# Kernel optimization log

Hardware: AMD Instinct MI355X
Metric: run time of the kernel (lower is better)

## Reference

```python
import jax, jax.numpy as jnp
import numpy as np

N_NODES = 50000
EMBED_DIM = 128
HIDDEN_DIM = 64
N_EDGES = 1600000
TEMP = 1.0


def setup_inputs() -> dict:
    key = jax.random.key(0)
    k1, k2, k3, k4 = jax.random.split(key, 4)
    node_embed = jax.random.normal(k1, (N_NODES, EMBED_DIM), dtype=jnp.float32)
    edge_index = jax.random.randint(k2, (2, N_EDGES), 0, N_NODES, dtype=jnp.int64)
    # MLP params (Linear(2*D, H) -> ReLU -> Linear(H, 1)); PyTorch-style fan-in scaling
    W1 = jax.random.normal(k3, (2 * EMBED_DIM, HIDDEN_DIM), dtype=jnp.float32) * (1.0 / np.sqrt(2 * EMBED_DIM))
    b1 = jnp.zeros((HIDDEN_DIM,), dtype=jnp.float32)
    W2 = jax.random.normal(k4, (HIDDEN_DIM, 1), dtype=jnp.float32) * (1.0 / np.sqrt(HIDDEN_DIM))
    b2 = jnp.zeros((1,), dtype=jnp.float32)
    return {"node_embed": node_embed, "edge_index": edge_index,
            "W1": W1, "b1": b1, "W2": W2, "b2": b2}


def reference(node_embed, edge_index, W1, b1, W2, b2):
    row, col = edge_index[0], edge_index[1]
    # gather + concat: [E, 2*D]
    edge_feat = jnp.concatenate([node_embed[row], node_embed[col]], axis=1)
    # tiny 2-layer MLP (dropout = identity in eval mode)
    h = jax.nn.relu(edge_feat @ W1 + b1)            # [E, H]
    edge_logits = (h @ W2 + b2)[:, 0]               # [E]
    # gumbel-sigmoid: difference of two Gumbel(0,1) samples (= logistic noise)
    nk = jax.random.key(42)
    nk1, nk2 = jax.random.split(nk)
    noise = jax.random.gumbel(nk1, edge_logits.shape, dtype=edge_logits.dtype) \
          - jax.random.gumbel(nk2, edge_logits.shape, dtype=edge_logits.dtype)
    edge_probs = jax.nn.sigmoid((edge_logits + noise) / TEMP)
    return edge_probs
```

## Files before the change

kernel.cpp:

```cpp
#include <hip/hip_runtime.h>
#include <hip/hip_bf16.h>
#include <stdint.h>

#define N_NODES 50000
#define NE      1600000
#define DIM     128
#define HID     64

typedef __attribute__((ext_vector_type(8))) short bf16x8;
typedef __attribute__((ext_vector_type(4))) float f32x4;

struct TF2 { uint32_t a, b; };

__host__ __device__ constexpr uint32_t rotl32(uint32_t x, int d) {
  return (x << d) | (x >> (32 - d));
}

__host__ __device__ constexpr TF2 threefry(uint32_t k0, uint32_t k1,
                                           uint32_t c0, uint32_t c1) {
  uint32_t ks[3] = { k0, k1, k0 ^ k1 ^ 0x1BD11BDAu };
  uint32_t x0 = c0 + ks[0], x1 = c1 + ks[1];
  const int rot[2][4] = { {13, 15, 26, 6}, {17, 29, 16, 24} };
  for (int i = 0; i < 5; ++i) {
    for (int r = 0; r < 4; ++r) {
      x0 += x1;
      x1 = rotl32(x1, rot[i & 1][r]);
      x1 ^= x0;
    }
    x0 += ks[(i + 1) % 3];
    x1 += ks[(i + 2) % 3] + (uint32_t)(i + 1);
  }
  return { x0, x1 };
}

constexpr TF2 SPA = threefry(0u, 42u, 0u, 0u);
constexpr TF2 SPB = threefry(0u, 42u, 0u, 1u);
constexpr uint32_t NK1_0 = SPA.a, NK1_1 = SPA.b;
constexpr uint32_t NK2_0 = SPB.a, NK2_1 = SPB.b;

__device__ inline float gumbel_elem(uint32_t k0, uint32_t k1, uint32_t i) {
  TF2 t = threefry(k0, k1, 0u, i);
  uint32_t bits = t.a ^ t.b;
  float f = __uint_as_float((bits >> 9) | 0x3f800000u) - 1.0f;
  float u = fmaxf(1.1754943508222875e-38f, f + 1.1754943508222875e-38f);
  return -__logf(-__logf(u));
}

__device__ inline unsigned short f2bf_rne(float f) {
  uint32_t u = __float_as_uint(f);
  uint32_t r = (u + 0x7fffu + ((u >> 16) & 1u)) >> 16;
  return (unsigned short)r;
}

#define NPB_M  64
#define NBLKN  ((N_NODES + NPB_M - 1) / NPB_M)
#define WT_LD  136

__global__ __launch_bounds__(256, 4)
void node_mfma_kernel(const float* __restrict__ node,
                      const float* __restrict__ W1,
                      const float* __restrict__ b1,
                      unsigned short* __restrict__ A_tab,
                      unsigned short* __restrict__ B_tab) {
  __shared__ unsigned short wt[128 * WT_LD];

  const int tid  = threadIdx.x;
  const int lane = tid & 63;
  const int w    = tid >> 6;
  const int c    = lane & 15;
  const int b    = lane >> 4;
  const int v0   = blockIdx.x * NPB_M;

  for (int idx = tid; idx < 128 * 128; idx += 256) {
    const int k  = idx >> 7;
    const int np = idx & 127;
    const float wv = W1[((size_t)((np >> 6) * 128 + k)) * HID + (np & 63)];
    wt[np * WT_LD + k] = f2bf_rne(wv);
  }
  __syncthreads();

  const int vld = min(v0 + w * 16 + c, N_NODES - 1);
  const float4* __restrict__ xrp = (const float4*)(node + (size_t)vld * DIM);
  float4 xx[8];
#pragma unroll
  for (int kk = 0; kk < 4; ++kk) {
    xx[2 * kk]     = xrp[kk * 8 + b * 2];
    xx[2 * kk + 1] = xrp[kk * 8 + b * 2 + 1];
  }

  f32x4 acc[8];
#pragma unroll
  for (int nt = 0; nt < 8; ++nt) acc[nt] = (f32x4){0.f, 0.f, 0.f, 0.f};

#pragma unroll
  for (int kk = 0; kk < 4; ++kk) {
    const float4 x0 = xx[2 * kk];
    const float4 x1 = xx[2 * kk + 1];
    const float xs[8] = { x0.x, x0.y, x0.z, x0.w, x1.x, x1.y, x1.z, x1.w };
    bf16x8 af;
#pragma unroll
    for (int j = 0; j < 8; ++j) af[j] = (short)f2bf_rne(xs[j]);

#pragma unroll
    for (int nt = 0; nt < 8; ++nt) {
      const bf16x8 bf =
          *(const bf16x8*)&wt[(nt * 16 + c) * WT_LD + kk * 32 + b * 8];
      acc[nt] = __builtin_amdgcn_mfma_f32_16x16x32_bf16(af, bf, acc[nt], 0, 0, 0);
    }
  }

#pragma unroll
  for (int nt = 0; nt < 8; ++nt) {
    const int np = nt * 16 + c;
    const float badd = (np < HID) ? b1[np] : 0.0f;
    unsigned short* __restrict__ base =
        (np < HID) ? (A_tab + np) : (B_tab + (np - HID));
#pragma unroll
    for (int r = 0; r < 4; ++r) {
      const int v = v0 + w * 16 + b * 4 + r;
      if (v < N_NODES) base[(size_t)v * HID] = f2bf_rne(acc[nt][r] + badd);
    }
  }
}

__global__ __launch_bounds__(256, 5)
void edge_kernel(const int* __restrict__ ei,
                 const unsigned short* __restrict__ A_tab,
                 const unsigned short* __restrict__ B_tab,
                 const float* __restrict__ W2,
                 const float* __restrict__ b2,
                 float* __restrict__ out) {
  const int tid    = blockIdx.x * blockDim.x + threadIdx.x;
  const int stride = gridDim.x * blockDim.x;
  const float bias2 = b2[0];

  for (int e = tid; e < NE; e += stride) {
    const int r = __builtin_nontemporal_load(ei + e);
    const int c = __builtin_nontemporal_load(ei + NE + e);
    const uint4* __restrict__ ap = (const uint4*)(A_tab + (size_t)r * HID);
    const uint4* __restrict__ bp = (const uint4*)(B_tab + (size_t)c * HID);

    uint4 av[8], bv[8];
#pragma unroll
    for (int q = 0; q < 8; ++q) av[q] = ap[q];
#pragma unroll
    for (int q = 0; q < 8; ++q) bv[q] = bp[q];

    float logit = bias2;
#pragma unroll
    for (int q = 0; q < 8; ++q) {
      const uint32_t* au = (const uint32_t*)&av[q];
      const uint32_t* bu = (const uint32_t*)&bv[q];
#pragma unroll
      for (int t = 0; t < 4; ++t) {
        const float a0 = __uint_as_float(au[t] << 16);
        const float a1 = __uint_as_float(au[t] & 0xffff0000u);
        const float b0 = __uint_as_float(bu[t] << 16);
        const float b1v = __uint_as_float(bu[t] & 0xffff0000u);
        const int jj = q * 8 + t * 2;
        logit = fmaf(fmaxf(a0 + b0, 0.0f),  W2[jj],     logit);
        logit = fmaf(fmaxf(a1 + b1v, 0.0f), W2[jj + 1], logit);
      }
    }

    const float g1 = gumbel_elem(NK1_0, NK1_1, (uint32_t)e);
    const float g2 = gumbel_elem(NK2_0, NK2_1, (uint32_t)e);
    const float z  = logit + g1 - g2;
    __builtin_nontemporal_store(1.0f / (1.0f + __expf(-z)), out + e);
  }
}

__global__ __launch_bounds__(256, 4)
void edge_prune_fallback(const float* __restrict__ node,
                         const int*   __restrict__ ei,
                         const float* __restrict__ W1,
                         const float* __restrict__ b1,
                         const float* __restrict__ W2,
                         const float* __restrict__ b2,
                         float*       __restrict__ out) {
  const int tid    = blockIdx.x * blockDim.x + threadIdx.x;
  const int stride = gridDim.x * blockDim.x;
  const float bias2 = b2[0];

  for (int e = tid; e < NE; e += stride) {
    const int r = ei[e];
    const int c = ei[NE + e];
    const float4* __restrict__ up = (const float4*)(node + (size_t)r * DIM);
    const float4* __restrict__ vp = (const float4*)(node + (size_t)c * DIM);

    float h[HID];
#pragma unroll
    for (int j = 0; j < HID; ++j) h[j] = b1[j];

#pragma unroll 1
    for (int dd = 0; dd < DIM / 4; ++dd) {
      const float4 xu = up[dd];
      const float4 xv = vp[dd];
      const float xs[8] = { xu.x, xu.y, xu.z, xu.w, xv.x, xv.y, xv.z, xv.w };
#pragma unroll
      for (int k = 0; k < 8; ++k) {
        const int drow = (k < 4) ? (dd * 4 + k) : (DIM + dd * 4 + (k - 4));
        const float4* __restrict__ wrow = (const float4*)(W1 + drow * HID);
        const float x = xs[k];
#pragma unroll
        for (int j4 = 0; j4 < HID / 4; ++j4) {
          const float4 w = wrow[j4];
          h[j4 * 4 + 0] = fmaf(x, w.x, h[j4 * 4 + 0]);
          h[j4 * 4 + 1] = fmaf(x, w.y, h[j4 * 4 + 1]);
          h[j4 * 4 + 2] = fmaf(x, w.z, h[j4 * 4 + 2]);
          h[j4 * 4 + 3] = fmaf(x, w.w, h[j4 * 4 + 3]);
        }
      }
    }

    float logit = bias2;
#pragma unroll
    for (int j = 0; j < HID; ++j) logit = fmaf(fmaxf(h[j], 0.0f), W2[j], logit);

    const float g1 = gumbel_elem(NK1_0, NK1_1, (uint32_t)e);
    const float g2 = gumbel_elem(NK2_0, NK2_1, (uint32_t)e);
    const float z  = logit + g1 - g2;
    out[e] = 1.0f / (1.0f + __expf(-z));
  }
}

extern "C" void kernel_launch(void* const* d_in, const int* in_sizes, int n_in,
                              void* d_out, int out_size, void* d_ws, size_t ws_size,
                              hipStream_t stream) {
  const float* node = (const float*)d_in[0];
  const int*   ei   = (const int*)  d_in[1];
  const float* W1   = (const float*)d_in[2];
  const float* b1   = (const float*)d_in[3];
  const float* W2   = (const float*)d_in[4];
  const float* b2   = (const float*)d_in[5];
  float* out = (float*)d_out;

  const size_t tab_bytes = (size_t)N_NODES * HID * sizeof(unsigned short);
  if (ws_size >= 2 * tab_bytes) {
    unsigned short* A_tab = (unsigned short*)d_ws;
    unsigned short* B_tab = A_tab + (size_t)N_NODES * HID;
    node_mfma_kernel<<<dim3(NBLKN), dim3(256), 0, stream>>>(
        node, W1, b1, A_tab, B_tab);
    edge_kernel<<<dim3(1280), dim3(256), 0, stream>>>(
        ei, A_tab, B_tab, W2, b2, out);
  } else {
    edge_prune_fallback<<<dim3(1024), dim3(256), 0, stream>>>(
        node, ei, W1, b1, W2, b2, out);
  }
}
```

Before: 84.14 us.

## Gather edge table rows into LDS via direct global-to-LDS DMA loads

Rewrites the edge kernel so each wave gathers the bf16 A/B table rows for 64 edges into shared memory with global_load_lds, coalescing one 16-byte segment per lane, using an XOR swizzle to avoid bank conflicts. Gumbel noise is computed while the loads are in flight, then the waits are drained and each lane reads its row from LDS. This replaces per-thread scattered 16-byte register loads with wave-cooperative loads that overlap the RNG arithmetic, at the cost of 64KB LDS per block, lower occupancy (2 blocks/CU) and a smaller grid with no cross-iteration prefetch.

```diff
diff --git a/kernel.cpp b/kernel.cpp
--- a/kernel.cpp
+++ b/kernel.cpp
@@ -123,49 +123,72 @@
   }
 }
 
-__global__ __launch_bounds__(256, 5)
-void edge_kernel(const int* __restrict__ ei,
-                 const unsigned short* __restrict__ A_tab,
-                 const unsigned short* __restrict__ B_tab,
-                 const float* __restrict__ W2,
-                 const float* __restrict__ b2,
-                 float* __restrict__ out) {
-  const int tid    = blockIdx.x * blockDim.x + threadIdx.x;
-  const int stride = gridDim.x * blockDim.x;
+#define EPB    256
+#define NBATCH (NE / EPB)
+
+__global__ __launch_bounds__(256, 2)
+void edge_kernel_dma(const int* __restrict__ ei,
+                     const unsigned short* __restrict__ A_tab,
+                     const unsigned short* __restrict__ B_tab,
+                     const float* __restrict__ W2,
+                     const float* __restrict__ b2,
+                     float* __restrict__ out) {
+  __shared__ uint4 buf[4096];
+
+  const int lane = threadIdx.x & 63;
+  const int w    = threadIdx.x >> 6;
+  const int l7   = lane & 7;
   const float bias2 = b2[0];
 
-  for (int e = tid; e < NE; e += stride) {
-    const int r = __builtin_nontemporal_load(ei + e);
-    const int c = __builtin_nontemporal_load(ei + NE + e);
-    const uint4* __restrict__ ap = (const uint4*)(A_tab + (size_t)r * HID);
-    const uint4* __restrict__ bp = (const uint4*)(B_tab + (size_t)c * HID);
-
-    uint4 av[8], bv[8];
-#pragma unroll
-    for (int q = 0; q < 8; ++q) av[q] = ap[q];
-#pragma unroll
-    for (int q = 0; q < 8; ++q) bv[q] = bp[q];
+  uint4* wbuf = buf + w * 1024;
+
+  for (int bt = blockIdx.x; bt < NBATCH; bt += gridDim.x) {
+    const int e0 = bt * EPB + w * 64;
+
+#pragma unroll
+    for (int j = 0; j < 16; ++j) {
+      const int sgl = j * 64 + lane;
+      const int ed  = sgl >> 4;
+      const int s   = sgl & 15;
+      const int q   = (s & 8) | ((s & 7) ^ (ed & 7));
+      const int idx = __builtin_nontemporal_load(ei + e0 + ed + (q < 8 ? 0 : NE));
+      const unsigned short* g =
+          (q < 8 ? A_tab : B_tab) + (size_t)idx * HID + (q & 7) * 8;
+      __builtin_amdgcn_global_load_lds(
+          (const __attribute__((address_space(1))) uint32_t*)g,
+          (__attribute__((address_space(3))) uint32_t*)(wbuf + j * 64),
+          16, 0, 0);
+    }
+
+    const int e = e0 + lane;
+    const float g1 = gumbel_elem(NK1_0, NK1_1, (uint32_t)e);
+    const float g2 = gumbel_elem(NK2_0, NK2_1, (uint32_t)e);
+
+    asm volatile("s_waitcnt vmcnt(0)" ::: "memory");
+    __builtin_amdgcn_sched_barrier(0);
 
     float logit = bias2;
-#pragma unroll
-    for (int q = 0; q < 8; ++q) {
-      const uint32_t* au = (const uint32_t*)&av[q];
-      const uint32_t* bu = (const uint32_t*)&bv[q];
+    const int tbase = lane * 16;
+#pragma unroll
+    for (int qq = 0; qq < 8; ++qq) {
+      const int slo = qq ^ l7;
+      const uint4 a4 = wbuf[tbase + slo];
+      const uint4 b4 = wbuf[tbase + 8 + slo];
+      const uint32_t* au = (const uint32_t*)&a4;
+      const uint32_t* bu = (const uint32_t*)&b4;
 #pragma unroll
       for (int t = 0; t < 4; ++t) {
         const float a0 = __uint_as_float(au[t] << 16);
         const float a1 = __uint_as_float(au[t] & 0xffff0000u);
         const float b0 = __uint_as_float(bu[t] << 16);
         const float b1v = __uint_as_float(bu[t] & 0xffff0000u);
-        const int jj = q * 8 + t * 2;
+        const int jj = qq * 8 + t * 2;
         logit = fmaf(fmaxf(a0 + b0, 0.0f),  W2[jj],     logit);
         logit = fmaf(fmaxf(a1 + b1v, 0.0f), W2[jj + 1], logit);
       }
     }
 
-    const float g1 = gumbel_elem(NK1_0, NK1_1, (uint32_t)e);
-    const float g2 = gumbel_elem(NK2_0, NK2_1, (uint32_t)e);
-    const float z  = logit + g1 - g2;
+    const float z = logit + g1 - g2;
     __builtin_nontemporal_store(1.0f / (1.0f + __expf(-z)), out + e);
   }
 }
@@ -241,7 +264,7 @@
     unsigned short* B_tab = A_tab + (size_t)N_NODES * HID;
     node_mfma_kernel<<<dim3(NBLKN), dim3(256), 0, stream>>>(
         node, W1, b1, A_tab, B_tab);
-    edge_kernel<<<dim3(1280), dim3(256), 0, stream>>>(
+    edge_kernel_dma<<<dim3(512), dim3(256), 0, stream>>>(
         ei, A_tab, B_tab, W2, b2, out);
   } else {
     edge_prune_fallback<<<dim3(1024), dim3(256), 0, stream>>>(
```

Result: faster. 67.94 us (-19.2%).
